# Kernel tuning notes

Measured on AMD Instinct MI355X. Metric: run time of the kernel, lower is better.

The kernel has to match this reference:

```python
import jax, jax.numpy as jnp
import numpy as np

KDIM = 128

def setup_inputs() -> dict:
    key = jax.random.key(0)
    kq, kk, kv = jax.random.split(key, 3)
    B, S, D = 8, 2048, KDIM
    q = jax.random.normal(kq, (B, S, D), dtype=jnp.float32)
    k = jax.random.normal(kk, (B, S, D), dtype=jnp.float32)
    v = jax.random.normal(kv, (B, S, D), dtype=jnp.float32)
    # causal mask: True = masked (future keys)
    mask = jnp.triu(jnp.ones((S, S), dtype=bool), k=1)
    return {"q": q, "k": k, "v": v, "mask": mask}

def reference(q, k, v, mask):
    # scores: [B, S_q, S_k]
    scores = jnp.einsum("bqd,bkd->bqk", q, k) / jnp.sqrt(jnp.asarray(KDIM, q.dtype))
    scores = jnp.where(mask, -jnp.inf, scores)
    attn = jax.nn.softmax(scores, axis=-1)
    return jnp.einsum("bqk,bkd->bqd", attn, v)
```

## Files before the change

### kernel.cpp

```cpp
#include <hip/hip_runtime.h>
#include <hip/hip_bf16.h>

#define S_LEN 2048
#define DHEAD 128

typedef __bf16 bf16x8 __attribute__((ext_vector_type(8)));
typedef float  f32x16 __attribute__((ext_vector_type(16)));

union PK { __bf16 h[2]; unsigned u; };
union BW { unsigned w4[4]; bf16x8 v; };

__device__ __forceinline__ bf16x8 cvt8(float4 a, float4 b) {
  bf16x8 r;
  r[0] = (__bf16)a.x; r[1] = (__bf16)a.y; r[2] = (__bf16)a.z; r[3] = (__bf16)a.w;
  r[4] = (__bf16)b.x; r[5] = (__bf16)b.y; r[6] = (__bf16)b.z; r[7] = (__bf16)b.w;
  return r;
}

#if __has_builtin(__builtin_amdgcn_permlane32_swap)
__device__ __forceinline__ void plswap(unsigned &a, unsigned &b) {
  auto r = __builtin_amdgcn_permlane32_swap((int)a, (int)b, false, false);
  a = (unsigned)r[0];
  b = (unsigned)r[1];
}
#else
__device__ __forceinline__ void plswap(unsigned &a, unsigned &b) {
  const bool hi = (threadIdx.x & 32) != 0;
  const unsigned ea = (unsigned)__shfl_xor((int)a, 32);
  const unsigned eb = (unsigned)__shfl_xor((int)b, 32);
  const unsigned na = hi ? eb : a;
  const unsigned nb = hi ? b : ea;
  a = na; b = nb;
}
#endif

__global__ __launch_bounds__(256) void kprep(const float* __restrict__ K,
                                             char* __restrict__ Kp) {
  const int tid = threadIdx.x;
  const int b = blockIdx.x >> 6;
  const int t = blockIdx.x & 63;
  const int row = tid >> 3;
  const int c8  = tid & 7;
  const float4* src = (const float4*)(K + ((size_t)(b * S_LEN + 32 * t + row) * DHEAD + 16 * c8));
  float4 f0 = src[0], f1 = src[1], f2 = src[2], f3 = src[3];
  char* dst = Kp + (size_t)(b * 64 + t) * 8192 + c8 * 1024 + row * 16;
  *(bf16x8*)(dst)       = cvt8(f0, f1);
  *(bf16x8*)(dst + 512) = cvt8(f2, f3);
}

__global__ __launch_bounds__(256) void vprep(const float* __restrict__ V,
                                             char* __restrict__ Vp) {
  __shared__ float t[32 * 132];
  const int tid = threadIdx.x;
  const int b = blockIdx.x >> 6;
  const int u = blockIdx.x & 63;
  const int row = tid >> 3;
  const int c8  = tid & 7;
  const float4* src = (const float4*)(V + ((size_t)(b * S_LEN + 32 * u + row) * DHEAD + 16 * c8));
  float4 f0 = src[0], f1 = src[1], f2 = src[2], f3 = src[3];
  float* d = t + row * 132 + 16 * c8;
  *(float4*)(d) = f0; *(float4*)(d + 4) = f1;
  *(float4*)(d + 8) = f2; *(float4*)(d + 12) = f3;
  __syncthreads();
#pragma unroll
  for (int k = 0; k < 2; ++k) {
    const int id = tid * 2 + k;
    const int lq = id & 31, hh = (id >> 5) & 1, s = (id >> 6) & 1, db = (id >> 7) & 3;
    bf16x8 o;
#pragma unroll
    for (int j = 0; j < 8; ++j) o[j] = (__bf16)t[(16 * s + 8 * hh + j) * 132 + 32 * db + lq];
    *(bf16x8*)(Vp + (size_t)(b * 64 + u) * 8192 + id * 16) = o;
  }
}

__global__ __launch_bounds__(256, 2) void attn_fwd(
    const float* __restrict__ Q, const char* __restrict__ Kp,
    const char* __restrict__ Vp, float* __restrict__ Out) {
  __shared__ __align__(16) char lds[38016];

  const int tid  = threadIdx.x;
  const int w    = tid >> 6;
  const int lane = tid & 63;
  const int h    = lane >> 5;
  const int lq   = lane & 31;

  const int bi    = blockIdx.x;
  const int batch = bi & 7;
  const int T     = (bi < 256) ? (63 - (bi >> 3)) : ((bi - 256) >> 3);
  const int q0    = T << 5;
  const int q     = q0 + lq;

  const float* Qb = Q + (size_t)batch * S_LEN * DHEAD;
  const char*  Kb = Kp + (size_t)batch * (S_LEN * 256) + h * 512 + lq * 16;
  const char*  Vb = Vp + (size_t)batch * (S_LEN * 256) + h * 512 + lq * 16;

  const float scale = 0.12751777903743892f;
  bf16x8 qf[8];
  {
    const float* qp = Qb + (size_t)q * DHEAD + 8 * h;
#pragma unroll
    for (int ks = 0; ks < 8; ++ks) {
      float4 a = *(const float4*)(qp + 16 * ks);
      float4 b = *(const float4*)(qp + 16 * ks + 4);
      a.x *= scale; a.y *= scale; a.z *= scale; a.w *= scale;
      b.x *= scale; b.y *= scale; b.z *= scale; b.w *= scale;
      qf[ks] = cvt8(a, b);
    }
  }

  float  mrun = -INFINITY, lrun = 0.f;
  f32x16 ob[4];
#pragma unroll
  for (int db = 0; db < 4; ++db)
#pragma unroll
    for (int r = 0; r < 16; ++r) ob[db][r] = 0.f;

  if (w <= T) {
    bf16x8 kf[8];
#pragma unroll
    for (int c = 0; c < 8; ++c) kf[c] = *(const bf16x8*)(Kb + w * 8192 + c * 1024);

    for (int u = w; u <= T; u += 4) {
      bf16x8 vf[8];
      const char* vb = Vb + u * 8192;
#pragma unroll
      for (int c = 0; c < 8; ++c) vf[c] = *(const bf16x8*)(vb + c * 1024);

      f32x16 sa, sb;
#pragma unroll
      for (int r = 0; r < 16; ++r) { sa[r] = 0.f; sb[r] = 0.f; }
      __builtin_amdgcn_s_setprio(1);
#pragma unroll
      for (int ks = 0; ks < 4; ++ks)
        sa = __builtin_amdgcn_mfma_f32_32x32x16_bf16(kf[ks], qf[ks], sa, 0, 0, 0);
#pragma unroll
      for (int ks = 4; ks < 8; ++ks)
        sb = __builtin_amdgcn_mfma_f32_32x32x16_bf16(kf[ks], qf[ks], sb, 0, 0, 0);
      __builtin_amdgcn_s_setprio(0);

      const int tn = (u + 4 <= T) ? (u + 4) : T;
      const char* kb2 = Kb + tn * 8192;
#pragma unroll
      for (int c = 0; c < 8; ++c) kf[c] = *(const bf16x8*)(kb2 + c * 1024);

      float sv[16];
#pragma unroll
      for (int r = 0; r < 16; ++r) sv[r] = sa[r] + sb[r];
      if (u == T) {
#pragma unroll
        for (int r = 0; r < 16; ++r) {
          const int kvr = (r & 3) + 8 * (r >> 2) + 4 * h;
          if (kvr > lq) sv[r] = -INFINITY;
        }
      }

      float mx = sv[0];
#pragma unroll
      for (int r = 1; r < 16; ++r) mx = fmaxf(mx, sv[r]);
      mx = fmaxf(mx, __shfl_xor(mx, 32));

      if (__any(mx > mrun + 12.f)) {
        const float mnew = fmaxf(mrun, mx);
        const float al = exp2f(mrun - mnew);
        lrun *= al;
#pragma unroll
        for (int db = 0; db < 4; ++db)
#pragma unroll
          for (int r = 0; r < 16; ++r) ob[db][r] *= al;
        mrun = mnew;
      }

      float pv[16];
      float rsum = 0.f;
#pragma unroll
      for (int r = 0; r < 16; ++r) {
        pv[r] = exp2f(sv[r] - mrun);
        rsum += pv[r];
      }
      lrun += rsum + __shfl_xor(rsum, 32);

      unsigned cc[8];
#pragma unroll
      for (int i = 0; i < 8; ++i) {
        PK pk;
        pk.h[0] = (__bf16)pv[2 * i];
        pk.h[1] = (__bf16)pv[2 * i + 1];
        cc[i] = pk.u;
      }
      plswap(cc[0], cc[2]); plswap(cc[1], cc[3]);
      plswap(cc[4], cc[6]); plswap(cc[5], cc[7]);
      BW pb0, pb1;
      pb0.w4[0] = cc[0]; pb0.w4[1] = cc[1]; pb0.w4[2] = cc[2]; pb0.w4[3] = cc[3];
      pb1.w4[0] = cc[4]; pb1.w4[1] = cc[5]; pb1.w4[2] = cc[6]; pb1.w4[3] = cc[7];

      __builtin_amdgcn_s_setprio(1);
#pragma unroll
      for (int db = 0; db < 4; ++db) {
        ob[db] = __builtin_amdgcn_mfma_f32_32x32x16_bf16(vf[2 * db],     pb0.v, ob[db], 0, 0, 0);
        ob[db] = __builtin_amdgcn_mfma_f32_32x32x16_bf16(vf[2 * db + 1], pb1.v, ob[db], 0, 0, 0);
      }
      __builtin_amdgcn_s_setprio(0);
    }
  }

  float2* ml   = (float2*)(lds + 36864);
  float*  Lbuf = (float*)(lds + 37888);
  float*  Ob0  = (float*)(lds);
  float*  Ob1  = (float*)(lds + 16896);

  if (h == 0) ml[w * 32 + lq] = make_float2(mrun, lrun);
  __syncthreads();

  float M = -INFINITY;
#pragma unroll
  for (int ww = 0; ww < 4; ++ww) M = fmaxf(M, ml[ww * 32 + lq].x);
  float L = 0.f;
#pragma unroll
  for (int ww = 0; ww < 4; ++ww) {
    float2 v = ml[ww * 32 + lq];
    L += v.y * exp2f(v.x - M);
  }
  const float fw = exp2f(mrun - M);
  if (w == 0 && h == 0) Lbuf[lq] = 1.f / L;

  float* Ob = (w & 1) ? Ob1 : Ob0;
  if (w < 2) {
#pragma unroll
    for (int db = 0; db < 4; ++db)
#pragma unroll
      for (int rr = 0; rr < 4; ++rr) {
        float4 val = { ob[db][4 * rr + 0] * fw, ob[db][4 * rr + 1] * fw,
                       ob[db][4 * rr + 2] * fw, ob[db][4 * rr + 3] * fw };
        *(float4*)(Ob + lq * 132 + 32 * db + 8 * rr + 4 * h) = val;
      }
  }
  __syncthreads();
  if (w >= 2) {
#pragma unroll
    for (int db = 0; db < 4; ++db)
#pragma unroll
      for (int rr = 0; rr < 4; ++rr) {
        float* p = Ob + lq * 132 + 32 * db + 8 * rr + 4 * h;
        float4 cur = *(float4*)p;
        cur.x += ob[db][4 * rr + 0] * fw;
        cur.y += ob[db][4 * rr + 1] * fw;
        cur.z += ob[db][4 * rr + 2] * fw;
        cur.w += ob[db][4 * rr + 3] * fw;
        *(float4*)p = cur;
      }
  }
  __syncthreads();

  const int row = tid >> 3;
  const int d0  = (tid & 7) * 16;
  const float inv = Lbuf[row];
  float* orow = Out + ((size_t)(batch * S_LEN + q0 + row)) * DHEAD + d0;
#pragma unroll
  for (int j = 0; j < 4; ++j) {
    float4 a = *(float4*)(Ob0 + row * 132 + d0 + 4 * j);
    float4 b = *(float4*)(Ob1 + row * 132 + d0 + 4 * j);
    float4 o = { (a.x + b.x) * inv, (a.y + b.y) * inv,
                 (a.z + b.z) * inv, (a.w + b.w) * inv };
    *(float4*)(orow + 4 * j) = o;
  }
}

extern "C" void kernel_launch(void* const* d_in, const int* in_sizes, int n_in,
                              void* d_out, int out_size, void* d_ws, size_t ws_size,
                              hipStream_t stream) {
  const float* q = (const float*)d_in[0];
  const float* k = (const float*)d_in[1];
  const float* v = (const float*)d_in[2];
  float* out = (float*)d_out;
  const int B = in_sizes[0] / (S_LEN * DHEAD);

  char* kp = (char*)d_ws;
  char* vp = (char*)d_ws + (size_t)B * S_LEN * 256;

  kprep<<<dim3(B * 64), dim3(256), 0, stream>>>(k, kp);
  vprep<<<dim3(B * 64), dim3(256), 0, stream>>>(v, vp);
  attn_fwd<<<dim3(B * (S_LEN / 32)), dim3(256), 0, stream>>>(q, kp, vp, out);
}
```

Baseline: 35.64 us.

## Fuse K/V prep kernels and pair causal tiles per 8-wave block

Measured after the change: 38.51 us. 1.08x slower.

```diff
diff --git a/kernel.cpp b/kernel.cpp
--- a/kernel.cpp
+++ b/kernel.cpp
@@ -9,6 +9,7 @@
 
 union PK { __bf16 h[2]; unsigned u; };
 union BW { unsigned w4[4]; bf16x8 v; };
+union FU { float f; unsigned u; };
 
 __device__ __forceinline__ bf16x8 cvt8(float4 a, float4 b) {
   bf16x8 r;
@@ -33,50 +34,56 @@
   a = na; b = nb;
 }
 #endif
-
-__global__ __launch_bounds__(256) void kprep(const float* __restrict__ K,
-                                             char* __restrict__ Kp) {
-  const int tid = threadIdx.x;
-  const int b = blockIdx.x >> 6;
-  const int t = blockIdx.x & 63;
-  const int row = tid >> 3;
-  const int c8  = tid & 7;
-  const float4* src = (const float4*)(K + ((size_t)(b * S_LEN + 32 * t + row) * DHEAD + 16 * c8));
-  float4 f0 = src[0], f1 = src[1], f2 = src[2], f3 = src[3];
-  char* dst = Kp + (size_t)(b * 64 + t) * 8192 + c8 * 1024 + row * 16;
-  *(bf16x8*)(dst)       = cvt8(f0, f1);
-  *(bf16x8*)(dst + 512) = cvt8(f2, f3);
-}
-
-__global__ __launch_bounds__(256) void vprep(const float* __restrict__ V,
-                                             char* __restrict__ Vp) {
+__device__ __forceinline__ float xmax32(float x) {
+  FU a, b; a.f = x; b.f = x; plswap(a.u, b.u); return fmaxf(a.f, b.f);
+}
+__device__ __forceinline__ float xsum32(float x) {
+  FU a, b; a.f = x; b.f = x; plswap(a.u, b.u); return a.f + b.f;
+}
+
+__global__ __launch_bounds__(256) void kvprep(const float* __restrict__ K,
+                                              const float* __restrict__ V,
+                                              char* __restrict__ Kp,
+                                              char* __restrict__ Vp, int nkb) {
   __shared__ float t[32 * 132];
   const int tid = threadIdx.x;
-  const int b = blockIdx.x >> 6;
-  const int u = blockIdx.x & 63;
-  const int row = tid >> 3;
-  const int c8  = tid & 7;
-  const float4* src = (const float4*)(V + ((size_t)(b * S_LEN + 32 * u + row) * DHEAD + 16 * c8));
-  float4 f0 = src[0], f1 = src[1], f2 = src[2], f3 = src[3];
-  float* d = t + row * 132 + 16 * c8;
-  *(float4*)(d) = f0; *(float4*)(d + 4) = f1;
-  *(float4*)(d + 8) = f2; *(float4*)(d + 12) = f3;
-  __syncthreads();
-#pragma unroll
-  for (int k = 0; k < 2; ++k) {
-    const int id = tid * 2 + k;
-    const int lq = id & 31, hh = (id >> 5) & 1, s = (id >> 6) & 1, db = (id >> 7) & 3;
-    bf16x8 o;
-#pragma unroll
-    for (int j = 0; j < 8; ++j) o[j] = (__bf16)t[(16 * s + 8 * hh + j) * 132 + 32 * db + lq];
-    *(bf16x8*)(Vp + (size_t)(b * 64 + u) * 8192 + id * 16) = o;
+  if ((int)blockIdx.x < nkb) {
+    const int bid = blockIdx.x;
+    const int b = bid >> 6, tt = bid & 63;
+    const int row = tid >> 3, c8 = tid & 7;
+    const float4* src = (const float4*)(K + ((size_t)(b * S_LEN + 32 * tt + row) * DHEAD + 16 * c8));
+    float4 f0 = src[0], f1 = src[1], f2 = src[2], f3 = src[3];
+    char* dst = Kp + (size_t)(b * 64 + tt) * 8192 + c8 * 1024 + row * 16;
+    *(bf16x8*)(dst)       = cvt8(f0, f1);
+    *(bf16x8*)(dst + 512) = cvt8(f2, f3);
+  } else {
+    const int bid = blockIdx.x - nkb;
+    const int b = bid >> 6, u = bid & 63;
+    const int row = tid >> 3, c8 = tid & 7;
+    const float4* src = (const float4*)(V + ((size_t)(b * S_LEN + 32 * u + row) * DHEAD + 16 * c8));
+    float4 f0 = src[0], f1 = src[1], f2 = src[2], f3 = src[3];
+    float* d = t + row * 132 + 16 * c8;
+    *(float4*)(d) = f0; *(float4*)(d + 4) = f1;
+    *(float4*)(d + 8) = f2; *(float4*)(d + 12) = f3;
+    __syncthreads();
+#pragma unroll
+    for (int k = 0; k < 2; ++k) {
+      const int id = tid * 2 + k;
+      const int lq = id & 31, hh = (id >> 5) & 1, s = (id >> 6) & 1, db = (id >> 7) & 3;
+      bf16x8 o;
+#pragma unroll
+      for (int j = 0; j < 8; ++j) o[j] = (__bf16)t[(16 * s + 8 * hh + j) * 132 + 32 * db + lq];
+      *(bf16x8*)(Vp + (size_t)(b * 64 + u) * 8192 + id * 16) = o;
+    }
   }
 }
 
-__global__ __launch_bounds__(256, 2) void attn_fwd(
+__global__ __launch_bounds__(512, 2) void attn_fwd(
     const float* __restrict__ Q, const char* __restrict__ Kp,
     const char* __restrict__ Vp, float* __restrict__ Out) {
-  __shared__ __align__(16) char lds[38016];
+  __shared__ __align__(16) char lds[71808];
+  float2* ml   = (float2*)(lds + 69632);
+  float*  Lbuf = (float*)(lds + 71680);
 
   const int tid  = threadIdx.x;
   const int w    = tid >> 6;
@@ -86,182 +93,194 @@
 
   const int bi    = blockIdx.x;
   const int batch = bi & 7;
-  const int T     = (bi < 256) ? (63 - (bi >> 3)) : ((bi - 256) >> 3);
-  const int q0    = T << 5;
-  const int q     = q0 + lq;
+  const int tp    = bi >> 3;
 
   const float* Qb = Q + (size_t)batch * S_LEN * DHEAD;
   const char*  Kb = Kp + (size_t)batch * (S_LEN * 256) + h * 512 + lq * 16;
   const char*  Vb = Vp + (size_t)batch * (S_LEN * 256) + h * 512 + lq * 16;
 
   const float scale = 0.12751777903743892f;
-  bf16x8 qf[8];
-  {
-    const float* qp = Qb + (size_t)q * DHEAD + 8 * h;
-#pragma unroll
-    for (int ks = 0; ks < 8; ++ks) {
-      float4 a = *(const float4*)(qp + 16 * ks);
-      float4 b = *(const float4*)(qp + 16 * ks + 4);
-      a.x *= scale; a.y *= scale; a.z *= scale; a.w *= scale;
-      b.x *= scale; b.y *= scale; b.z *= scale; b.w *= scale;
-      qf[ks] = cvt8(a, b);
-    }
-  }
-
-  float  mrun = -INFINITY, lrun = 0.f;
-  f32x16 ob[4];
-#pragma unroll
-  for (int db = 0; db < 4; ++db)
-#pragma unroll
-    for (int r = 0; r < 16; ++r) ob[db][r] = 0.f;
-
-  if (w <= T) {
-    bf16x8 kf[8];
-#pragma unroll
-    for (int c = 0; c < 8; ++c) kf[c] = *(const bf16x8*)(Kb + w * 8192 + c * 1024);
-
-    for (int u = w; u <= T; u += 4) {
-      bf16x8 vf[8];
-      const char* vb = Vb + u * 8192;
-#pragma unroll
-      for (int c = 0; c < 8; ++c) vf[c] = *(const bf16x8*)(vb + c * 1024);
-
-      f32x16 sa, sb;
-#pragma unroll
-      for (int r = 0; r < 16; ++r) { sa[r] = 0.f; sb[r] = 0.f; }
-      __builtin_amdgcn_s_setprio(1);
-#pragma unroll
-      for (int ks = 0; ks < 4; ++ks)
-        sa = __builtin_amdgcn_mfma_f32_32x32x16_bf16(kf[ks], qf[ks], sa, 0, 0, 0);
-#pragma unroll
-      for (int ks = 4; ks < 8; ++ks)
-        sb = __builtin_amdgcn_mfma_f32_32x32x16_bf16(kf[ks], qf[ks], sb, 0, 0, 0);
-      __builtin_amdgcn_s_setprio(0);
-
-      const int tn = (u + 4 <= T) ? (u + 4) : T;
-      const char* kb2 = Kb + tn * 8192;
-#pragma unroll
-      for (int c = 0; c < 8; ++c) kf[c] = *(const bf16x8*)(kb2 + c * 1024);
-
-      float sv[16];
-#pragma unroll
-      for (int r = 0; r < 16; ++r) sv[r] = sa[r] + sb[r];
-      if (u == T) {
-#pragma unroll
-        for (int r = 0; r < 16; ++r) {
-          const int kvr = (r & 3) + 8 * (r >> 2) + 4 * h;
-          if (kvr > lq) sv[r] = -INFINITY;
-        }
+
+#pragma unroll 1
+  for (int ph = 0; ph < 2; ++ph) {
+    const int T  = ph ? tp : (63 - tp);
+    const int q0 = T << 5;
+
+    bf16x8 qf[8];
+    {
+      const float* qp = Qb + (size_t)(q0 + lq) * DHEAD + 8 * h;
+#pragma unroll
+      for (int ks = 0; ks < 8; ++ks) {
+        float4 a = *(const float4*)(qp + 16 * ks);
+        float4 b = *(const float4*)(qp + 16 * ks + 4);
+        a.x *= scale; a.y *= scale; a.z *= scale; a.w *= scale;
+        b.x *= scale; b.y *= scale; b.z *= scale; b.w *= scale;
+        qf[ks] = cvt8(a, b);
       }
-
-      float mx = sv[0];
-#pragma unroll
-      for (int r = 1; r < 16; ++r) mx = fmaxf(mx, sv[r]);
-      mx = fmaxf(mx, __shfl_xor(mx, 32));
-
-      if (__any(mx > mrun + 12.f)) {
-        const float mnew = fmaxf(mrun, mx);
-        const float al = exp2f(mrun - mnew);
-        lrun *= al;
-#pragma unroll
-        for (int db = 0; db < 4; ++db)
-#pragma unroll
-          for (int r = 0; r < 16; ++r) ob[db][r] *= al;
-        mrun = mnew;
+    }
+
+    float  mrun = -INFINITY, lrun = 0.f;
+    f32x16 ob[4];
+#pragma unroll
+    for (int db = 0; db < 4; ++db)
+#pragma unroll
+      for (int r = 0; r < 16; ++r) ob[db][r] = 0.f;
+
+    if (w <= T) {
+      bf16x8 kf[8];
+#pragma unroll
+      for (int c = 0; c < 8; ++c) kf[c] = *(const bf16x8*)(Kb + w * 8192 + c * 1024);
+
+      for (int u = w; u <= T; u += 8) {
+        bf16x8 vf[8];
+        const char* vb = Vb + u * 8192;
+#pragma unroll
+        for (int c = 0; c < 8; ++c) vf[c] = *(const bf16x8*)(vb + c * 1024);
+
+        f32x16 sa, sb;
+#pragma unroll
+        for (int r = 0; r < 16; ++r) { sa[r] = 0.f; sb[r] = 0.f; }
+        __builtin_amdgcn_s_setprio(1);
+#pragma unroll
+        for (int ks = 0; ks < 4; ++ks)
+          sa = __builtin_amdgcn_mfma_f32_32x32x16_bf16(kf[ks], qf[ks], sa, 0, 0, 0);
+#pragma unroll
+        for (int ks = 4; ks < 8; ++ks)
+          sb = __builtin_amdgcn_mfma_f32_32x32x16_bf16(kf[ks], qf[ks], sb, 0, 0, 0);
+        __builtin_amdgcn_s_setprio(0);
+
+        const int tn = (u + 8 <= T) ? (u + 8) : T;
+        const char* kb2 = Kb + tn * 8192;
+#pragma unroll
+        for (int c = 0; c < 8; ++c) kf[c] = *(const bf16x8*)(kb2 + c * 1024);
+
+        float sv[16];
+#pragma unroll
+        for (int r = 0; r < 16; ++r) sv[r] = sa[r] + sb[r];
+        if (u == T) {
+#pragma unroll
+          for (int r = 0; r < 16; ++r) {
+            const int kvr = (r & 3) + 8 * (r >> 2) + 4 * h;
+            if (kvr > lq) sv[r] = -INFINITY;
+          }
+        }
+
+        float m8[8];
+#pragma unroll
+        for (int r = 0; r < 8; ++r) m8[r] = fmaxf(sv[r], sv[r + 8]);
+#pragma unroll
+        for (int r = 0; r < 4; ++r) m8[r] = fmaxf(m8[r], m8[r + 4]);
+        float mx = fmaxf(fmaxf(m8[0], m8[1]), fmaxf(m8[2], m8[3]));
+        mx = xmax32(mx);
+
+        if (__any(mx > mrun + 12.f)) {
+          const float mnew = fmaxf(mrun, mx);
+          const float al = exp2f(mrun - mnew);
+          lrun *= al;
+#pragma unroll
+          for (int db = 0; db < 4; ++db)
+#pragma unroll
+            for (int r = 0; r < 16; ++r) ob[db][r] *= al;
+          mrun = mnew;
+        }
+
+        float pv[16];
+#pragma unroll
+        for (int r = 0; r < 16; ++r) pv[r] = exp2f(sv[r] - mrun);
+        float s8[8];
+#pragma unroll
+        for (int r = 0; r < 8; ++r) s8[r] = pv[r] + pv[r + 8];
+#pragma unroll
+        for (int r = 0; r < 4; ++r) s8[r] = s8[r] + s8[r + 4];
+        lrun += xsum32((s8[0] + s8[1]) + (s8[2] + s8[3]));
+
+        unsigned cc[8];
+#pragma unroll
+        for (int i = 0; i < 8; ++i) {
+          PK pk;
+          pk.h[0] = (__bf16)pv[2 * i];
+          pk.h[1] = (__bf16)pv[2 * i + 1];
+          cc[i] = pk.u;
+        }
+        plswap(cc[0], cc[2]); plswap(cc[1], cc[3]);
+        plswap(cc[4], cc[6]); plswap(cc[5], cc[7]);
+        BW pb0, pb1;
+        pb0.w4[0] = cc[0]; pb0.w4[1] = cc[1]; pb0.w4[2] = cc[2]; pb0.w4[3] = cc[3];
+        pb1.w4[0] = cc[4]; pb1.w4[1] = cc[5]; pb1.w4[2] = cc[6]; pb1.w4[3] = cc[7];
+
+        __builtin_amdgcn_s_setprio(1);
+#pragma unroll
+        for (int db = 0; db < 4; ++db) {
+          ob[db] = __builtin_amdgcn_mfma_f32_32x32x16_bf16(vf[2 * db],     pb0.v, ob[db], 0, 0, 0);
+          ob[db] = __builtin_amdgcn_mfma_f32_32x32x16_bf16(vf[2 * db + 1], pb1.v, ob[db], 0, 0, 0);
+        }
+        __builtin_amdgcn_s_setprio(0);
       }
-
-      float pv[16];
-      float rsum = 0.f;
-#pragma unroll
-      for (int r = 0; r < 16; ++r) {
-        pv[r] = exp2f(sv[r] - mrun);
-        rsum += pv[r];
-      }
-      lrun += rsum + __shfl_xor(rsum, 32);
-
-      unsigned cc[8];
-#pragma unroll
-      for (int i = 0; i < 8; ++i) {
-        PK pk;
-        pk.h[0] = (__bf16)pv[2 * i];
-        pk.h[1] = (__bf16)pv[2 * i + 1];
-        cc[i] = pk.u;
-      }
-      plswap(cc[0], cc[2]); plswap(cc[1], cc[3]);
-      plswap(cc[4], cc[6]); plswap(cc[5], cc[7]);
-      BW pb0, pb1;
-      pb0.w4[0] = cc[0]; pb0.w4[1] = cc[1]; pb0.w4[2] = cc[2]; pb0.w4[3] = cc[3];
-      pb1.w4[0] = cc[4]; pb1.w4[1] = cc[5]; pb1.w4[2] = cc[6]; pb1.w4[3] = cc[7];
-
-      __builtin_amdgcn_s_setprio(1);
-#pragma unroll
-      for (int db = 0; db < 4; ++db) {
-        ob[db] = __builtin_amdgcn_mfma_f32_32x32x16_bf16(vf[2 * db],     pb0.v, ob[db], 0, 0, 0);
-        ob[db] = __builtin_amdgcn_mfma_f32_32x32x16_bf16(vf[2 * db + 1], pb1.v, ob[db], 0, 0, 0);
-      }
-      __builtin_amdgcn_s_setprio(0);
-    }
-  }
-
-  float2* ml   = (float2*)(lds + 36864);
-  float*  Lbuf = (float*)(lds + 37888);
-  float*  Ob0  = (float*)(lds);
-  float*  Ob1  = (float*)(lds + 16896);
-
-  if (h == 0) ml[w * 32 + lq] = make_float2(mrun, lrun);
-  __syncthreads();
-
-  float M = -INFINITY;
-#pragma unroll
-  for (int ww = 0; ww < 4; ++ww) M = fmaxf(M, ml[ww * 32 + lq].x);
-  float L = 0.f;
-#pragma unroll
-  for (int ww = 0; ww < 4; ++ww) {
-    float2 v = ml[ww * 32 + lq];
-    L += v.y * exp2f(v.x - M);
-  }
-  const float fw = exp2f(mrun - M);
-  if (w == 0 && h == 0) Lbuf[lq] = 1.f / L;
-
-  float* Ob = (w & 1) ? Ob1 : Ob0;
-  if (w < 2) {
-#pragma unroll
-    for (int db = 0; db < 4; ++db)
-#pragma unroll
-      for (int rr = 0; rr < 4; ++rr) {
-        float4 val = { ob[db][4 * rr + 0] * fw, ob[db][4 * rr + 1] * fw,
-                       ob[db][4 * rr + 2] * fw, ob[db][4 * rr + 3] * fw };
-        *(float4*)(Ob + lq * 132 + 32 * db + 8 * rr + 4 * h) = val;
-      }
-  }
-  __syncthreads();
-  if (w >= 2) {
-#pragma unroll
-    for (int db = 0; db < 4; ++db)
-#pragma unroll
-      for (int rr = 0; rr < 4; ++rr) {
-        float* p = Ob + lq * 132 + 32 * db + 8 * rr + 4 * h;
-        float4 cur = *(float4*)p;
-        cur.x += ob[db][4 * rr + 0] * fw;
-        cur.y += ob[db][4 * rr + 1] * fw;
-        cur.z += ob[db][4 * rr + 2] * fw;
-        cur.w += ob[db][4 * rr + 3] * fw;
-        *(float4*)p = cur;
-      }
-  }
-  __syncthreads();
-
-  const int row = tid >> 3;
-  const int d0  = (tid & 7) * 16;
-  const float inv = Lbuf[row];
-  float* orow = Out + ((size_t)(batch * S_LEN + q0 + row)) * DHEAD + d0;
-#pragma unroll
-  for (int j = 0; j < 4; ++j) {
-    float4 a = *(float4*)(Ob0 + row * 132 + d0 + 4 * j);
-    float4 b = *(float4*)(Ob1 + row * 132 + d0 + 4 * j);
-    float4 o = { (a.x + b.x) * inv, (a.y + b.y) * inv,
-                 (a.z + b.z) * inv, (a.w + b.w) * inv };
-    *(float4*)(orow + 4 * j) = o;
+    }
+
+    __syncthreads();
+    if (h == 0) ml[w * 32 + lq] = make_float2(mrun, lrun);
+    __syncthreads();
+
+    float M = -INFINITY;
+#pragma unroll
+    for (int ww = 0; ww < 8; ++ww) M = fmaxf(M, ml[ww * 32 + lq].x);
+    float L = 0.f;
+#pragma unroll
+    for (int ww = 0; ww < 8; ++ww) {
+      float2 v = ml[ww * 32 + lq];
+      L += v.y * exp2f(v.x - M);
+    }
+    const float fw = exp2f(mrun - M);
+    if (w == 0 && h == 0) Lbuf[lq] = 1.f / L;
+
+    float* Obw = (float*)(lds + (w & 3) * 17408);
+    if (w < 4) {
+#pragma unroll
+      for (int db = 0; db < 4; ++db)
+#pragma unroll
+        for (int rr = 0; rr < 4; ++rr) {
+          float4 val = { ob[db][4 * rr + 0] * fw, ob[db][4 * rr + 1] * fw,
+                         ob[db][4 * rr + 2] * fw, ob[db][4 * rr + 3] * fw };
+          *(float4*)(Obw + lq * 136 + 32 * db + 8 * rr + 4 * h) = val;
+        }
+    }
+    __syncthreads();
+    if (w >= 4) {
+#pragma unroll
+      for (int db = 0; db < 4; ++db)
+#pragma unroll
+        for (int rr = 0; rr < 4; ++rr) {
+          float* p = Obw + lq * 136 + 32 * db + 8 * rr + 4 * h;
+          float4 cur = *(float4*)p;
+          cur.x += ob[db][4 * rr + 0] * fw;
+          cur.y += ob[db][4 * rr + 1] * fw;
+          cur.z += ob[db][4 * rr + 2] * fw;
+          cur.w += ob[db][4 * rr + 3] * fw;
+          *(float4*)p = cur;
+        }
+    }
+    __syncthreads();
+
+    const int row = tid >> 4;
+    const int d0  = (tid & 15) * 8;
+    const float inv = Lbuf[row];
+    const float* O0 = (const float*)(lds);
+    const float* O1 = (const float*)(lds + 17408);
+    const float* O2 = (const float*)(lds + 34816);
+    const float* O3 = (const float*)(lds + 52224);
+    float* orow = Out + ((size_t)(batch * S_LEN + q0 + row)) * DHEAD + d0;
+#pragma unroll
+    for (int j = 0; j < 2; ++j) {
+      const int off = row * 136 + d0 + 4 * j;
+      float4 a = *(const float4*)(O0 + off);
+      float4 b = *(const float4*)(O1 + off);
+      float4 c = *(const float4*)(O2 + off);
+      float4 d = *(const float4*)(O3 + off);
+      float4 o = { (a.x + b.x + c.x + d.x) * inv, (a.y + b.y + c.y + d.y) * inv,
+                   (a.z + b.z + c.z + d.z) * inv, (a.w + b.w + c.w + d.w) * inv };
+      *(float4*)(orow + 4 * j) = o;
+    }
   }
 }
 
@@ -277,7 +296,6 @@
   char* kp = (char*)d_ws;
   char* vp = (char*)d_ws + (size_t)B * S_LEN * 256;
 
-  kprep<<<dim3(B * 64), dim3(256), 0, stream>>>(k, kp);
-  vprep<<<dim3(B * 64), dim3(256), 0, stream>>>(v, vp);
-  attn_fwd<<<dim3(B * (S_LEN / 32)), dim3(256), 0, stream>>>(q, kp, vp, out);
-}
+  kvprep<<<dim3(B * 128), dim3(256), 0, stream>>>(k, v, kp, vp, B * 64);
+  attn_fwd<<<dim3(B * 32), dim3(512), 0, stream>>>(q, kp, vp, out);
+}
```
